# Kernel tuning notes

Hardware: AMD Instinct MI355X
Metric: run time of the kernel (lower is better)

## Reference

```python
import math
import jax, jax.numpy as jnp
import numpy as np

B, S, D, H = 1, 4096, 1024, 16
HD = D // H


def setup_inputs() -> dict:
    key = jax.random.key(0)
    ks = jax.random.split(key, 11)
    s = 0.02
    inp = {
        "q": jax.random.normal(ks[0], (B, S, D), jnp.float32),
        "k": jax.random.normal(ks[1], (B, S, D), jnp.float32),
        "v": jax.random.normal(ks[2], (B, S, D), jnp.float32),
        # causal boolean mask, broadcastable over [B, H, S, S]
        "mask": jnp.tril(jnp.ones((S, S), jnp.bool_))[None, None],
        "Wq": jax.random.normal(ks[3], (D, D), jnp.float32) * s,
        "bq": jnp.zeros((D,), jnp.float32),
        "Wk": jax.random.normal(ks[4], (D, D), jnp.float32) * s,
        "bk": jnp.zeros((D,), jnp.float32),
        "Wv": jax.random.normal(ks[5], (D, D), jnp.float32) * s,
        "bv": jnp.zeros((D,), jnp.float32),
        "Wo": jax.random.normal(ks[6], (D, D), jnp.float32) * s,
        "bo": jnp.zeros((D,), jnp.float32),
    }
    return inp


def reference(q, k, v, mask, Wq, bq, Wk, bk, Wv, bv, Wo, bo):
    # projections (torch Linear: x @ W.T + b; here W is stored already transposed)
    qp = (q @ Wq + bq).reshape(B, S, H, HD)
    kp = (k @ Wk + bk).reshape(B, S, H, HD)
    vp = (v @ Wv + bv).reshape(B, S, H, HD)
    # scores: [B, H, S, S]
    scores = jnp.einsum("bqhd,bkhd->bhqk", qp, kp) / math.sqrt(HD)
    scores = jnp.where(mask, scores, -jnp.inf)
    attn = jax.nn.softmax(scores, axis=-1)
    # context: [B, H, S, HD] -> [B, S, D]
    ctx = jnp.einsum("bhqk,bkhd->bqhd", attn, vp).reshape(B, S, D)
    return ctx @ Wo + bo
```

## Files before the change

kernel.cpp:

```cpp
#include <hip/hip_runtime.h>
#include <hip/hip_bf16.h>


#define S_LEN 4096
#define D_DIM 1024
#define NHEAD 16
#define HDIM  64

typedef __hip_bfloat16 bf16;
typedef __attribute__((ext_vector_type(8))) short bf16x8v;
typedef __attribute__((ext_vector_type(4))) float f32x4;
typedef __attribute__((ext_vector_type(2))) unsigned int u32x2;

#define MFMA16(a, b, c) __builtin_amdgcn_mfma_f32_16x16x32_bf16((a), (b), (c), 0, 0, 0)

#if __has_builtin(__builtin_amdgcn_exp2f)
#define EXP2F(x) __builtin_amdgcn_exp2f(x)
#else
#define EXP2F(x) exp2f(x)
#endif

#define QSCALE (0.125f * 1.4426950408889634f)

__device__ __forceinline__ void async_cp16(const void* g, void* l) {
    __builtin_amdgcn_global_load_lds(
        (const __attribute__((address_space(1))) unsigned int*)g,
        (__attribute__((address_space(3))) unsigned int*)l, 16, 0, 0);
}

__device__ __forceinline__ unsigned int cvtpk_bf16(float lo, float hi) {
    unsigned int r;
    asm("v_cvt_pk_bf16_f32 %0, %1, %2" : "=v"(r) : "v"(lo), "v"(hi));
    return r;
}

__global__ __launch_bounds__(256) void cvt_bf16_k(
    const float* __restrict__ x0, const float* __restrict__ x1,
    const float* __restrict__ x2,
    bf16* __restrict__ y0, bf16* __restrict__ y1, bf16* __restrict__ y2)
{
    const float* x = (blockIdx.z == 0) ? x0 : (blockIdx.z == 1) ? x1 : x2;
    bf16*       y = (blockIdx.z == 0) ? y0 : (blockIdx.z == 1) ? y1 : y2;
    const size_t i = ((size_t)blockIdx.x * 256 + threadIdx.x);
    const float4 v = ((const float4*)x)[i];
    union { bf16 h[4]; short4 s; } u;
    u.h[0] = __float2bfloat16(v.x);
    u.h[1] = __float2bfloat16(v.y);
    u.h[2] = __float2bfloat16(v.z);
    u.h[3] = __float2bfloat16(v.w);
    ((short4*)y)[i] = u.s;
}

__global__ __launch_bounds__(256) void transpose_cvt_k(
    const float* __restrict__ W0, const float* __restrict__ W1,
    const float* __restrict__ W2, const float* __restrict__ W3,
    bf16* __restrict__ T0, bf16* __restrict__ T1,
    bf16* __restrict__ T2, bf16* __restrict__ T3)
{
    const float* W = (blockIdx.z == 0) ? W0 : (blockIdx.z == 1) ? W1
                   : (blockIdx.z == 2) ? W2 : W3;
    bf16*       Wt = (blockIdx.z == 0) ? T0 : (blockIdx.z == 1) ? T1
                   : (blockIdx.z == 2) ? T2 : T3;
    __shared__ float t[32][33];
    const int bx = blockIdx.x << 5, by = blockIdx.y << 5;
    const int tx = threadIdx.x & 31, ty = threadIdx.x >> 5;
#pragma unroll
    for (int i = 0; i < 32; i += 8)
        t[ty + i][tx] = W[(size_t)(by + ty + i) * D_DIM + bx + tx];
    __syncthreads();
#pragma unroll
    for (int i = 0; i < 32; i += 8)
        Wt[(size_t)(bx + ty + i) * D_DIM + by + tx] = __float2bfloat16(t[tx][ty + i]);
}

struct GemmJob {
    const bf16* A; const bf16* Wt; const float* bias; void* out;
    int mode; float scale;
};

__global__ __launch_bounds__(256) void gemm_k(GemmJob j0, GemmJob j1, GemmJob j2)
{
    const GemmJob j = (blockIdx.z == 0) ? j0 : (blockIdx.z == 1) ? j1 : j2;
    const int K = D_DIM;
    const int bn = blockIdx.x << 6;
    const int bm = blockIdx.y << 7;
    const int tid = threadIdx.x;
    const int w = tid >> 6, lane = tid & 63;
    const int col = lane & 15, g = lane >> 4;
    const int wr = (w >> 1) << 6, wc = (w & 1) << 5;

    __shared__ bf16 As[128 * 64];
    __shared__ bf16 Bs[64 * 64];

    f32x4 acc[4][2];
#pragma unroll
    for (int i = 0; i < 4; ++i)
#pragma unroll
        for (int jj = 0; jj < 2; ++jj) acc[i][jj] = (f32x4){0.f, 0.f, 0.f, 0.f};

    for (int kb = 0; kb < K; kb += 64) {
        __syncthreads();
#pragma unroll
        for (int e = 0; e < 4; ++e) {
            const int lin = (e << 8) + tid;
            const int row = lin >> 3, kc = lin & 7;
            async_cp16(j.A + (size_t)(bm + row) * K + kb + (kc << 3), &As[lin << 3]);
        }
#pragma unroll
        for (int e = 0; e < 2; ++e) {
            const int lin = (e << 8) + tid;
            const int row = lin >> 3, kc = lin & 7;
            async_cp16(j.Wt + (size_t)(bn + row) * K + kb + (kc << 3), &Bs[lin << 3]);
        }
        __syncthreads();

#pragma unroll
        for (int s = 0; s < 2; ++s) {
            bf16x8v af[4], bfv[2];
#pragma unroll
            for (int i = 0; i < 4; ++i)
                af[i] = *(const bf16x8v*)&As[((wr + (i << 4) + col) << 6) + (s << 5) + (g << 3)];
#pragma unroll
            for (int jj = 0; jj < 2; ++jj)
                bfv[jj] = *(const bf16x8v*)&Bs[((wc + (jj << 4) + col) << 6) + (s << 5) + (g << 3)];
#pragma unroll
            for (int i = 0; i < 4; ++i)
#pragma unroll
                for (int jj = 0; jj < 2; ++jj)
                    acc[i][jj] = MFMA16(af[i], bfv[jj], acc[i][jj]);
        }
    }

#pragma unroll
    for (int i = 0; i < 4; ++i)
#pragma unroll
    for (int jj = 0; jj < 2; ++jj)
#pragma unroll
    for (int reg = 0; reg < 4; ++reg) {
        const int row = bm + wr + (i << 4) + (g << 2) + reg;
        const int cg  = bn + wc + (jj << 4) + col;
        const float vv = (acc[i][jj][reg] + j.bias[cg]) * j.scale;
        if (j.mode == 0)
            ((bf16*)j.out)[(((size_t)(cg >> 6)) * S_LEN + row) * HDIM + (cg & 63)] =
                __float2bfloat16(vv);
        else if (j.mode == 2)
            ((bf16*)j.out)[((size_t)(cg >> 6) * HDIM + (cg & 63)) * S_LEN + row] =
                __float2bfloat16(vv);
        else
            ((float*)j.out)[(size_t)row * D_DIM + cg] = vv;
    }
}

__global__ __launch_bounds__(256) void attn_mfma_k(
    const bf16* __restrict__ Qp, const bf16* __restrict__ Kp,
    const bf16* __restrict__ Vt, bf16* __restrict__ ctx)
{
    __shared__ bf16 Ks[2][4096];
    __shared__ bf16 Vs[2][4096];

    const int bid = blockIdx.x;
    const int qb  = 63 - (bid >> 4);
    const int h   = bid & 15;
    const int q0  = qb << 6;
    const int tid = threadIdx.x, w = tid >> 6, lane = tid & 63;
    const int col = lane & 15, g = lane >> 4;

    const bf16* Kh = Kp + (size_t)h * S_LEN * HDIM;
    const bf16* Vh = Vt + (size_t)h * HDIM * S_LEN;

    const int qrow = q0 + (w << 4) + col;
    const size_t qrow_base = ((size_t)h * S_LEN + qrow) * HDIM + (g << 3);
    const bf16x8v qf0 = *(const bf16x8v*)(Qp + qrow_base);
    const bf16x8v qf1 = *(const bf16x8v*)(Qp + qrow_base + 32);

    float pl = 0.f;
    f32x4 acco[4];
#pragma unroll
    for (int t = 0; t < 4; ++t) acco[t] = (f32x4){0.f, 0.f, 0.f, 0.f};

    const int nkb = qb + 1;

    auto stage = [&](int buf, int kb) {
        const int kk0 = kb << 6;
#pragma unroll
        for (int e = 0; e < 2; ++e) {
            const int lin = (e << 8) + tid;
            const int t = lin >> 7, G = (lin >> 4) & 7, c = lin & 15;
            async_cp16(Kh + (size_t)(kk0 + (t << 4) + c) * HDIM + (G << 3),
                       &Ks[buf][lin << 3]);
            async_cp16(Vh + (size_t)((t << 4) + c) * S_LEN + kk0 + (G << 3),
                       &Vs[buf][lin << 3]);
        }
    };

    stage(0, 0);
    __syncthreads();

    for (int kb = 0; kb < nkb; ++kb) {
        const int cur = kb & 1;
        if (kb + 1 < nkb) stage(cur ^ 1, kb + 1);
        const int kk0 = kb << 6;
        const bf16* Kc = Ks[cur];
        const bf16* Vc = Vs[cur];

        f32x4 sa[4];
#pragma unroll
        for (int t = 0; t < 4; ++t) sa[t] = (f32x4){0.f, 0.f, 0.f, 0.f};
        __builtin_amdgcn_s_setprio(1);
#pragma unroll
        for (int t = 0; t < 4; ++t) {
            sa[t] = MFMA16(*(const bf16x8v*)&Kc[((t << 7) + (g << 4) + col) << 3], qf0, sa[t]);
            sa[t] = MFMA16(*(const bf16x8v*)&Kc[((t << 7) + 64 + (g << 4) + col) << 3], qf1, sa[t]);
        }
        __builtin_amdgcn_s_setprio(0);

        const bool lastt = (kb == nkb - 1);
#pragma unroll
        for (int t = 0; t < 4; ++t) {
#pragma unroll
            for (int reg = 0; reg < 4; ++reg) {
                const int kidx = kk0 + (t << 4) + (g << 2) + reg;
                float p;
                if (lastt && kidx > qrow)
                    p = 0.f;
                else
                    p = EXP2F(sa[t][reg]);
                pl += p;
                sa[t][reg] = p;
            }
        }

        unsigned int c0[4], c1[4];
#pragma unroll
        for (int t = 0; t < 4; ++t) {
            c0[t] = cvtpk_bf16(sa[t][0], sa[t][1]);
            c1[t] = cvtpk_bf16(sa[t][2], sa[t][3]);
        }
        union { unsigned int wd[4]; bf16x8v v; } pb0, pb1;
        {
            u32x2 r0 = __builtin_amdgcn_permlane32_swap(c0[0], c0[1], false, false);
            u32x2 r1 = __builtin_amdgcn_permlane32_swap(c1[0], c1[1], false, false);
            u32x2 s0 = __builtin_amdgcn_permlane16_swap(r0[0], r0[1], false, false);
            u32x2 s1 = __builtin_amdgcn_permlane16_swap(r1[0], r1[1], false, false);
            pb0.wd[0] = s0[0]; pb0.wd[1] = s1[0]; pb0.wd[2] = s0[1]; pb0.wd[3] = s1[1];
        }
        {
            u32x2 r0 = __builtin_amdgcn_permlane32_swap(c0[2], c0[3], false, false);
            u32x2 r1 = __builtin_amdgcn_permlane32_swap(c1[2], c1[3], false, false);
            u32x2 s0 = __builtin_amdgcn_permlane16_swap(r0[0], r0[1], false, false);
            u32x2 s1 = __builtin_amdgcn_permlane16_swap(r1[0], r1[1], false, false);
            pb1.wd[0] = s0[0]; pb1.wd[1] = s1[0]; pb1.wd[2] = s0[1]; pb1.wd[3] = s1[1];
        }

        __builtin_amdgcn_s_setprio(1);
#pragma unroll
        for (int t = 0; t < 4; ++t) {
            acco[t] = MFMA16(*(const bf16x8v*)&Vc[((t << 7) + (g << 4) + col) << 3], pb0.v, acco[t]);
            acco[t] = MFMA16(*(const bf16x8v*)&Vc[((t << 7) + 64 + (g << 4) + col) << 3], pb1.v, acco[t]);
        }
        __builtin_amdgcn_s_setprio(0);

        __syncthreads();
    }

    float l = pl;
    l += __shfl_xor(l, 16);
    l += __shfl_xor(l, 32);
    const float inv = 1.f / l;

#pragma unroll
    for (int t = 0; t < 4; ++t) {
        union { bf16 hh[4]; short4 s4; } u;
#pragma unroll
        for (int reg = 0; reg < 4; ++reg)
            u.hh[reg] = __float2bfloat16(acco[t][reg] * inv);
        *(short4*)&ctx[(size_t)qrow * D_DIM + h * HDIM + (t << 4) + (g << 2)] = u.s4;
    }
}

extern "C" void kernel_launch(void* const* d_in, const int* in_sizes, int n_in,
                              void* d_out, int out_size, void* d_ws, size_t ws_size,
                              hipStream_t stream)
{
    const float* q  = (const float*)d_in[0];
    const float* k  = (const float*)d_in[1];
    const float* v  = (const float*)d_in[2];
    const float* Wq = (const float*)d_in[4];
    const float* bq = (const float*)d_in[5];
    const float* Wk = (const float*)d_in[6];
    const float* bk = (const float*)d_in[7];
    const float* Wv = (const float*)d_in[8];
    const float* bv = (const float*)d_in[9];
    const float* Wo = (const float*)d_in[10];
    const float* bo = (const float*)d_in[11];

    const size_t PE  = (size_t)S_LEN * D_DIM;
    const size_t WTE = (size_t)D_DIM * D_DIM;

    const dim3 tg(32, 32, 4);
    const dim3 gg(D_DIM / 64, S_LEN / 128, 1);
    const dim3 gg3(D_DIM / 64, S_LEN / 128, 3);
    const dim3 cg((unsigned)(PE / 1024), 1, 3);

    if (ws_size >= (size_t)64 * 1024 * 1024) {
        bf16* Qb = (bf16*)d_ws;
        bf16* Kb = Qb + PE;
        bf16* Vb = Kb + PE;
        bf16* Qp = Vb + PE;
        bf16* Kp = Qp + PE;
        bf16* Vt = Kp + PE;
        bf16* Wtq = Vt + PE;
        bf16* Wtk = Wtq + WTE;
        bf16* Wtv = Wtk + WTE;
        bf16* Wto = Wtv + WTE;
        bf16* ctx = Qb;

        transpose_cvt_k<<<tg, 256, 0, stream>>>(Wq, Wk, Wv, Wo, Wtq, Wtk, Wtv, Wto);
        cvt_bf16_k<<<cg, 256, 0, stream>>>(q, k, v, Qb, Kb, Vb);

        GemmJob jq{Qb, Wtq, bq, Qp, 0, QSCALE};
        GemmJob jk{Kb, Wtk, bk, Kp, 0, 1.0f};
        GemmJob jv{Vb, Wtv, bv, Vt, 2, 1.0f};
        gemm_k<<<gg3, 256, 0, stream>>>(jq, jk, jv);

        attn_mfma_k<<<dim3(1024), 256, 0, stream>>>(Qp, Kp, Vt, ctx);

        GemmJob jo{ctx, Wto, bo, d_out, 1, 1.0f};
        gemm_k<<<gg, 256, 0, stream>>>(jo, jo, jo);
    } else {
        bf16* X  = (bf16*)d_ws;
        bf16* Qp = X + PE;
        bf16* Kp = Qp + PE;
        bf16* Vt = Kp + PE;
        bf16* Wtq = Vt + PE;
        bf16* Wtk = Wtq + WTE;
        bf16* Wtv = Wtk + WTE;
        bf16* Wto = Wtv + WTE;

        transpose_cvt_k<<<tg, 256, 0, stream>>>(Wq, Wk, Wv, Wo, Wtq, Wtk, Wtv, Wto);

        const dim3 cg1((unsigned)(PE / 1024), 1, 1);
        cvt_bf16_k<<<cg1, 256, 0, stream>>>(q, q, q, X, X, X);
        GemmJob jq{X, Wtq, bq, Qp, 0, QSCALE};
        gemm_k<<<gg, 256, 0, stream>>>(jq, jq, jq);
        cvt_bf16_k<<<cg1, 256, 0, stream>>>(k, k, k, X, X, X);
        GemmJob jk{X, Wtk, bk, Kp, 0, 1.0f};
        gemm_k<<<gg, 256, 0, stream>>>(jk, jk, jk);
        cvt_bf16_k<<<cg1, 256, 0, stream>>>(v, v, v, X, X, X);
        GemmJob jv{X, Wtv, bv, Vt, 2, 1.0f};
        gemm_k<<<gg, 256, 0, stream>>>(jv, jv, jv);

        attn_mfma_k<<<dim3(1024), 256, 0, stream>>>(Qp, Kp, Vt, X);

        GemmJob jo{X, Wto, bo, d_out, 1, 1.0f};
        gemm_k<<<gg, 256, 0, stream>>>(jo, jo, jo);
    }
}
```

Before: 322.9 us.

## Split long causal query blocks across two KV chunks and drop double buffering

Query blocks in the upper half of the sequence are now split into two KV ranges that are processed by separate workgroups. Their unnormalized partial outputs and row sums are written to fp32 scratch, and a new combine kernel merges them. This balances the causal workload across 1536 blocks instead of 1024 and shortens the longest per-block tail. At the same time, the double-buffered async KV staging is replaced by a single buffer with a sync after each load, so loads no longer overlap compute. The change also adds an extra kernel launch and fp32 partial traffic.

After: 322.2 us. About the same (-0.2%).

```diff
diff --git a/kernel.cpp b/kernel.cpp
--- a/kernel.cpp
+++ b/kernel.cpp
@@ -153,14 +153,27 @@
 
 __global__ __launch_bounds__(256) void attn_mfma_k(
     const bf16* __restrict__ Qp, const bf16* __restrict__ Kp,
-    const bf16* __restrict__ Vt, bf16* __restrict__ ctx)
-{
-    __shared__ bf16 Ks[2][4096];
-    __shared__ bf16 Vs[2][4096];
+    const bf16* __restrict__ Vt, bf16* __restrict__ ctx,
+    float* __restrict__ Opart, float* __restrict__ lpart, int mode)
+{
+    __shared__ bf16 Ks[4096];
+    __shared__ bf16 Vs[4096];
 
     const int bid = blockIdx.x;
-    const int qb  = 63 - (bid >> 4);
     const int h   = bid & 15;
+    const int jid = bid >> 4;
+
+    int qb, t0, nt, chunk;
+    bool dosplit;
+    if (mode == 1) {
+        const int i3 = jid / 3, r = jid - i3 * 3;
+        if (r == 0)      { qb = 32 + i3; t0 = 0;  nt = 32;      dosplit = true;  chunk = 0; }
+        else if (r == 1) { qb = 31 - i3; t0 = 0;  nt = qb + 1;  dosplit = false; chunk = 0; }
+        else             { qb = 63 - i3; t0 = 32; nt = qb - 31; dosplit = true;  chunk = 1; }
+    } else {
+        qb = 63 - jid; t0 = 0; nt = qb + 1; dosplit = false; chunk = 0;
+    }
+
     const int q0  = qb << 6;
     const int tid = threadIdx.x, w = tid >> 6, lane = tid & 63;
     const int col = lane & 15, g = lane >> 4;
@@ -178,30 +191,18 @@
 #pragma unroll
     for (int t = 0; t < 4; ++t) acco[t] = (f32x4){0.f, 0.f, 0.f, 0.f};
 
-    const int nkb = qb + 1;
-
-    auto stage = [&](int buf, int kb) {
+    for (int kb = t0; kb < t0 + nt; ++kb) {
         const int kk0 = kb << 6;
 #pragma unroll
         for (int e = 0; e < 2; ++e) {
             const int lin = (e << 8) + tid;
             const int t = lin >> 7, G = (lin >> 4) & 7, c = lin & 15;
             async_cp16(Kh + (size_t)(kk0 + (t << 4) + c) * HDIM + (G << 3),
-                       &Ks[buf][lin << 3]);
+                       &Ks[lin << 3]);
             async_cp16(Vh + (size_t)((t << 4) + c) * S_LEN + kk0 + (G << 3),
-                       &Vs[buf][lin << 3]);
-        }
-    };
-
-    stage(0, 0);
-    __syncthreads();
-
-    for (int kb = 0; kb < nkb; ++kb) {
-        const int cur = kb & 1;
-        if (kb + 1 < nkb) stage(cur ^ 1, kb + 1);
-        const int kk0 = kb << 6;
-        const bf16* Kc = Ks[cur];
-        const bf16* Vc = Vs[cur];
+                       &Vs[lin << 3]);
+        }
+        __syncthreads();
 
         f32x4 sa[4];
 #pragma unroll
@@ -209,19 +210,19 @@
         __builtin_amdgcn_s_setprio(1);
 #pragma unroll
         for (int t = 0; t < 4; ++t) {
-            sa[t] = MFMA16(*(const bf16x8v*)&Kc[((t << 7) + (g << 4) + col) << 3], qf0, sa[t]);
-            sa[t] = MFMA16(*(const bf16x8v*)&Kc[((t << 7) + 64 + (g << 4) + col) << 3], qf1, sa[t]);
+            sa[t] = MFMA16(*(const bf16x8v*)&Ks[((t << 7) + (g << 4) + col) << 3], qf0, sa[t]);
+            sa[t] = MFMA16(*(const bf16x8v*)&Ks[((t << 7) + 64 + (g << 4) + col) << 3], qf1, sa[t]);
         }
         __builtin_amdgcn_s_setprio(0);
 
-        const bool lastt = (kb == nkb - 1);
+        const bool maskt = (kb == qb);
 #pragma unroll
         for (int t = 0; t < 4; ++t) {
 #pragma unroll
             for (int reg = 0; reg < 4; ++reg) {
                 const int kidx = kk0 + (t << 4) + (g << 2) + reg;
                 float p;
-                if (lastt && kidx > qrow)
+                if (maskt && kidx > qrow)
                     p = 0.f;
                 else
                     p = EXP2F(sa[t][reg]);
@@ -255,8 +256,8 @@
         __builtin_amdgcn_s_setprio(1);
 #pragma unroll
         for (int t = 0; t < 4; ++t) {
-            acco[t] = MFMA16(*(const bf16x8v*)&Vc[((t << 7) + (g << 4) + col) << 3], pb0.v, acco[t]);
-            acco[t] = MFMA16(*(const bf16x8v*)&Vc[((t << 7) + 64 + (g << 4) + col) << 3], pb1.v, acco[t]);
+            acco[t] = MFMA16(*(const bf16x8v*)&Vs[((t << 7) + (g << 4) + col) << 3], pb0.v, acco[t]);
+            acco[t] = MFMA16(*(const bf16x8v*)&Vs[((t << 7) + 64 + (g << 4) + col) << 3], pb1.v, acco[t]);
         }
         __builtin_amdgcn_s_setprio(0);
 
@@ -266,16 +267,47 @@
     float l = pl;
     l += __shfl_xor(l, 16);
     l += __shfl_xor(l, 32);
-    const float inv = 1.f / l;
-
-#pragma unroll
-    for (int t = 0; t < 4; ++t) {
-        union { bf16 hh[4]; short4 s4; } u;
-#pragma unroll
-        for (int reg = 0; reg < 4; ++reg)
-            u.hh[reg] = __float2bfloat16(acco[t][reg] * inv);
-        *(short4*)&ctx[(size_t)qrow * D_DIM + h * HDIM + (t << 4) + (g << 2)] = u.s4;
-    }
+
+    if (!dosplit) {
+        const float inv = 1.f / l;
+#pragma unroll
+        for (int t = 0; t < 4; ++t) {
+            union { bf16 hh[4]; short4 s4; } u;
+#pragma unroll
+            for (int reg = 0; reg < 4; ++reg)
+                u.hh[reg] = __float2bfloat16(acco[t][reg] * inv);
+            *(short4*)&ctx[(size_t)qrow * D_DIM + h * HDIM + (t << 4) + (g << 2)] = u.s4;
+        }
+    } else {
+        const int srow = ((qb - 32) << 6) + (w << 4) + col;
+        float* Op = Opart + (((size_t)chunk * NHEAD + h) * 2048 + srow) * HDIM;
+#pragma unroll
+        for (int t = 0; t < 4; ++t)
+            *(f32x4*)&Op[(t << 4) + (g << 2)] = acco[t];
+        if (g == 0)
+            lpart[((size_t)chunk * NHEAD + h) * 2048 + srow] = l;
+    }
+}
+
+__global__ __launch_bounds__(256) void combine_k(
+    const float* __restrict__ Opart, const float* __restrict__ lpart,
+    bf16* __restrict__ ctx)
+{
+    const int tid = threadIdx.x;
+    const int row = (blockIdx.x << 4) + (tid >> 4);
+    const int d4  = (tid & 15) << 2;
+    const int h   = row >> 11;
+    const int srow = row & 2047;
+    const float4 a = *(const float4*)&Opart[(size_t)row * HDIM + d4];
+    const float4 b = *(const float4*)&Opart[(size_t)(32768 + row) * HDIM + d4];
+    const float inv = 1.f / (lpart[row] + lpart[32768 + row]);
+    union { bf16 hh[4]; short4 s4; } u;
+    u.hh[0] = __float2bfloat16((a.x + b.x) * inv);
+    u.hh[1] = __float2bfloat16((a.y + b.y) * inv);
+    u.hh[2] = __float2bfloat16((a.z + b.z) * inv);
+    u.hh[3] = __float2bfloat16((a.w + b.w) * inv);
+    const int qrow = 2048 + srow;
+    *(short4*)&ctx[(size_t)qrow * D_DIM + h * HDIM + d4] = u.s4;
 }
 
 extern "C" void kernel_launch(void* const* d_in, const int* in_sizes, int n_in,
@@ -314,6 +346,8 @@
         bf16* Wtv = Wtk + WTE;
         bf16* Wto = Wtv + WTE;
         bf16* ctx = Qb;
+        float* Opart = (float*)Kb;
+        float* lpart = (float*)(Wto + WTE);
 
         transpose_cvt_k<<<tg, 256, 0, stream>>>(Wq, Wk, Wv, Wo, Wtq, Wtk, Wtv, Wto);
         cvt_bf16_k<<<cg, 256, 0, stream>>>(q, k, v, Qb, Kb, Vb);
@@ -323,7 +357,8 @@
         GemmJob jv{Vb, Wtv, bv, Vt, 2, 1.0f};
         gemm_k<<<gg3, 256, 0, stream>>>(jq, jk, jv);
 
-        attn_mfma_k<<<dim3(1024), 256, 0, stream>>>(Qp, Kp, Vt, ctx);
+        attn_mfma_k<<<dim3(1536), 256, 0, stream>>>(Qp, Kp, Vt, ctx, Opart, lpart, 1);
+        combine_k<<<dim3(2048), 256, 0, stream>>>(Opart, lpart, ctx);
 
         GemmJob jo{ctx, Wto, bo, d_out, 1, 1.0f};
         gemm_k<<<gg, 256, 0, stream>>>(jo, jo, jo);
@@ -350,7 +385,7 @@
         GemmJob jv{X, Wtv, bv, Vt, 2, 1.0f};
         gemm_k<<<gg, 256, 0, stream>>>(jv, jv, jv);
 
-        attn_mfma_k<<<dim3(1024), 256, 0, stream>>>(Qp, Kp, Vt, X);
+        attn_mfma_k<<<dim3(1024), 256, 0, stream>>>(Qp, Kp, Vt, X, nullptr, nullptr, 0);
 
         GemmJob jo{X, Wto, bo, d_out, 1, 1.0f};
         gemm_k<<<gg, 256, 0, stream>>>(jo, jo, jo);
```
